# Optimization experiments

Measured on AMD Instinct MI355X. Metric: run time of the kernel, lower is better.

The kernel has to match this reference:

```python
import jax, jax.numpy as jnp
import numpy as np

N_EMBD = 1024
NUM_HEADS = 16
HEAD_SIZE = N_EMBD // NUM_HEADS
B, T = 2, 2048


def setup_inputs() -> dict:
    key = jax.random.key(0)
    k1, k2, k3, k4 = jax.random.split(key, 4)
    x = jax.random.normal(k1, (B, T, N_EMBD), dtype=jnp.float32)
    # torch nn.Linear weight is [out,in]; we store transposed [in,out] for x @ W
    w_qkv = jax.random.normal(k2, (N_EMBD, 3 * N_EMBD), dtype=jnp.float32) * (N_EMBD ** -0.5)
    w_proj = jax.random.normal(k3, (N_EMBD, N_EMBD), dtype=jnp.float32) * (N_EMBD ** -0.5)
    b_proj = jax.random.normal(k4, (N_EMBD,), dtype=jnp.float32) * 0.01
    return {"x": x, "w_qkv": w_qkv, "w_proj": w_proj, "b_proj": b_proj}


def reference(x, w_qkv, w_proj, b_proj):
    Bm, Tm, C = x.shape
    H, D = NUM_HEADS, HEAD_SIZE
    qkv = x @ w_qkv  # [B,T,3C]
    # einops 'b t (h d three) -> three b h t d': 'three' is the innermost factor
    qkv = qkv.reshape(Bm, Tm, H, D, 3)
    q = qkv[..., 0].transpose(0, 2, 1, 3)  # [B,H,T,D]
    k = qkv[..., 1].transpose(0, 2, 1, 3)
    v = qkv[..., 2].transpose(0, 2, 1, 3)
    scale = D ** -0.5
    attn = jnp.einsum('bhqd,bhkd->bhqk', q, k) * scale  # [B,H,T,T]
    causal_mask = jnp.triu(jnp.ones((Tm, Tm), dtype=bool), k=1)
    attn = jnp.where(causal_mask, -jnp.inf, attn)
    attn = jax.nn.softmax(attn, axis=-1)
    out = jnp.einsum('bhqk,bhkd->bhqd', attn, v)  # [B,H,T,D]
    out = out.transpose(0, 2, 1, 3).reshape(Bm, Tm, C)  # b h t d -> b t (h d)
    out = out @ w_proj + b_proj
    return out
```

## Files before the change

kernel.cpp:

```cpp
#include <hip/hip_runtime.h>
#include <hip/hip_bf16.h>
#include <math.h>

typedef __bf16 bf16x8 __attribute__((ext_vector_type(8)));
typedef __bf16 bf16x4 __attribute__((ext_vector_type(4)));
typedef float f32x4 __attribute__((ext_vector_type(4)));

#define MFMA16(A, B, C) __builtin_amdgcn_mfma_f32_16x16x32_bf16(A, B, C, 0, 0, 0)

__device__ __forceinline__ void cp16(void* lds_base, const void* g) {
  __builtin_amdgcn_global_load_lds(
      (const __attribute__((address_space(1))) void*)g,
      (__attribute__((address_space(3))) void*)lds_base, 16, 0, 0);
}

static constexpr int Bc   = 2;
static constexpr int Tc   = 2048;
static constexpr int Cc   = 1024;
static constexpr int Hc   = 16;
static constexpr int Dc   = 64;
static constexpr int Mrows = Bc * Tc;
static constexpr int N3    = 3 * Cc;

__global__ __launch_bounds__(256) void convert_x(
    const float* __restrict__ src, __bf16* __restrict__ dst, int n) {
  const int i0 = (blockIdx.x * 256 + threadIdx.x) * 8;
  if (i0 >= n) return;
  f32x4 a = *(const f32x4*)(src + i0);
  f32x4 b = *(const f32x4*)(src + i0 + 4);
  bf16x8 v;
#pragma unroll
  for (int j = 0; j < 4; ++j) { v[j] = (__bf16)a[j]; v[4 + j] = (__bf16)b[j]; }
  *(bf16x8*)(dst + i0) = v;
}

__global__ __launch_bounds__(256) void transpose_weights(
    const float* __restrict__ wqkv, const float* __restrict__ wproj,
    __bf16* __restrict__ dqkv, __bf16* __restrict__ dproj) {
  __shared__ __bf16 tile[32][33];
  const bool isproj = blockIdx.x >= 96;
  const float* src = isproj ? wproj : wqkv;
  __bf16* dst = isproj ? dproj : dqkv;
  const int N = isproj ? Cc : N3;
  const int K = Cc;
  const int n0 = (isproj ? (blockIdx.x - 96) : blockIdx.x) * 32;
  const int k0 = blockIdx.y * 32;
  const int x = threadIdx.x & 31;
  const int y = threadIdx.x >> 5;
  {
    int n = n0 + x;
    int col = n;
    if (!isproj) {
      int three = n >> 10, rem = n & 1023;
      int h = rem >> 6, d = rem & 63;
      col = h * 192 + d * 3 + three;
    }
#pragma unroll
    for (int r = 0; r < 4; ++r) {
      int k = k0 + y + r * 8;
      tile[y + r * 8][x] = (__bf16)src[(size_t)k * N + col];
    }
  }
  __syncthreads();
#pragma unroll
  for (int r = 0; r < 4; ++r) {
    int n = n0 + y + r * 8;
    dst[(size_t)n * K + k0 + x] = tile[x][y + r * 8];
  }
}

__global__ __launch_bounds__(256) void v_transpose(
    const __bf16* __restrict__ qkvp, __bf16* __restrict__ vt) {
  __shared__ __bf16 tile[32][33];
  const int t0 = blockIdx.x * 32;
  const int d0 = blockIdx.y * 32;
  const int bh = blockIdx.z;
  const int b = bh >> 4, h = bh & 15;
  const int x = threadIdx.x & 31;
  const int y = threadIdx.x >> 5;
#pragma unroll
  for (int r = 0; r < 4; ++r) {
    int t = t0 + y + r * 8;
    tile[y + r * 8][x] =
        qkvp[(size_t)(b * Tc + t) * N3 + 2 * Cc + h * 64 + d0 + x];
  }
  __syncthreads();
#pragma unroll
  for (int r = 0; r < 4; ++r) {
    int d = d0 + y + r * 8;
    vt[((size_t)bh * 64 + d) * Tc + t0 + x] = tile[x][y + r * 8];
  }
}

template <bool F32OUT>
__global__ __launch_bounds__(256) void gemm_nt(
    const __bf16* __restrict__ A, const __bf16* __restrict__ Bt,
    void* __restrict__ Cmat, const float* __restrict__ bias,
    int M, int N, int K, int ldc) {
  __shared__ __align__(16) __bf16 As[128 * 64];
  __shared__ __align__(16) __bf16 Bs[128 * 64];
  const int n0 = blockIdx.x * 128, m0 = blockIdx.y * 128;
  const int tid = threadIdx.x;
  const int wave = tid >> 6, lane = tid & 63;
  const int quad = lane >> 4, l16 = lane & 15;
  const int wm = (wave >> 1) * 64, wn = (wave & 1) * 64;
  const int srow = lane >> 3;
  const int scol = (((lane & 7) ^ (srow & 7))) * 8;

  f32x4 acc[4][4] = {};

  for (int k0 = 0; k0 < K; k0 += 64) {
    __syncthreads();
#pragma unroll
    for (int c = 0; c < 4; ++c) {
      int rowblk = c * 4 + wave;
      int row = rowblk * 8 + srow;
      cp16(&As[rowblk * 512], A + (size_t)(m0 + row) * K + k0 + scol);
      cp16(&Bs[rowblk * 512], Bt + (size_t)(n0 + row) * K + k0 + scol);
    }
    __syncthreads();
#pragma unroll
    for (int kk = 0; kk < 64; kk += 32) {
      bf16x8 af[4], bfr[4];
#pragma unroll
      for (int i = 0; i < 4; ++i) {
        int chunk = (((kk >> 3) + quad) ^ (l16 & 7)) * 8;
        af[i]  = *(const bf16x8*)(&As[(wm + i * 16 + l16) * 64 + chunk]);
        bfr[i] = *(const bf16x8*)(&Bs[(wn + i * 16 + l16) * 64 + chunk]);
      }
#pragma unroll
      for (int mi = 0; mi < 4; ++mi)
#pragma unroll
        for (int ni = 0; ni < 4; ++ni)
          acc[mi][ni] = MFMA16(af[mi], bfr[ni], acc[mi][ni]);
    }
  }

#pragma unroll
  for (int ni = 0; ni < 4; ++ni) {
    int col = n0 + wn + ni * 16 + l16;
    float bv = bias ? bias[col] : 0.0f;
#pragma unroll
    for (int mi = 0; mi < 4; ++mi)
#pragma unroll
      for (int r = 0; r < 4; ++r) {
        int row = m0 + wm + mi * 16 + quad * 4 + r;
        float v = acc[mi][ni][r] + bv;
        if (F32OUT)
          ((float*)Cmat)[(size_t)row * ldc + col] = v;
        else
          ((__bf16*)Cmat)[(size_t)row * ldc + col] = (__bf16)v;
      }
  }
}

#define LOG2E 1.44269504088896340736f
#define C2SC  (0.125f * LOG2E)
#define SH2   (16.0f * LOG2E)
static constexpr int LPK = 72;
static constexpr int LPV = 136;
static constexpr int TB  = 128;

__global__ __launch_bounds__(512, 4) void attn_kernel(
    const __bf16* __restrict__ qkv,
    const __bf16* __restrict__ vt,
    __bf16* __restrict__ obuf) {
  __shared__ __align__(16) __bf16 Ks[TB * LPK];
  __shared__ __align__(16) __bf16 Vs[64 * LPV];
  __shared__ __align__(16) __bf16 plds[8][16 * LPK];

  const int bh = blockIdx.x;
  const int pairidx = blockIdx.y;
  const int b = bh >> 4, hh = bh & 15;
  const int tid = threadIdx.x;
  const int wave = tid >> 6, lane = tid & 63;
  const int quad = lane >> 4, l16 = lane & 15;

  const __bf16* qbase = qkv + (size_t)(b * Tc) * N3 + hh * 64;
  const __bf16* kbase = qbase + Cc;
  const __bf16* vtb = vt + (size_t)bh * 64 * Tc;

  const int krow = tid >> 2;
  const int kcol = (tid & 3) * 16;
  const int vrow = tid >> 3;
  const int vcol = (tid & 7) * 16;

#pragma unroll
  for (int pi = 0; pi < 2; ++pi) {
    const int qt = pi ? (15 - pairidx) : pairidx;
    const int q0 = qt * 128;
    const int qb = q0 + wave * 16;
    const int kblocks = q0 + 128;

    bf16x8 bQ[2];
    {
      const __bf16* qr = qbase + (size_t)(qb + l16) * N3;
      bQ[0] = *(const bf16x8*)(qr + quad * 8);
      bQ[1] = *(const bf16x8*)(qr + 32 + quad * 8);
    }

    f32x4 accO[4] = {};
    float l_part = 0.0f;

    bf16x8 kp[2], vp[2];
    {
      const __bf16* kr = kbase + (size_t)krow * N3 + kcol;
      const __bf16* vr = vtb + (size_t)vrow * Tc + vcol;
#pragma unroll
      for (int j = 0; j < 2; ++j) {
        kp[j] = *(const bf16x8*)(kr + j * 8);
        vp[j] = *(const bf16x8*)(vr + j * 8);
      }
    }

    for (int kc = 0; kc < kblocks; kc += TB) {
      __syncthreads();
#pragma unroll
      for (int j = 0; j < 2; ++j) {
        *(bf16x8*)(&Ks[krow * LPK + kcol + j * 8]) = kp[j];
        *(bf16x8*)(&Vs[vrow * LPV + vcol + j * 8]) = vp[j];
      }
      if (kc + TB < kblocks) {
        const __bf16* kr = kbase + (size_t)(kc + TB + krow) * N3 + kcol;
        const __bf16* vr = vtb + (size_t)vrow * Tc + kc + TB + vcol;
#pragma unroll
        for (int j = 0; j < 2; ++j) {
          kp[j] = *(const bf16x8*)(kr + j * 8);
          vp[j] = *(const bf16x8*)(vr + j * 8);
        }
      }
      __syncthreads();

#pragma unroll
      for (int sub = 0; sub < 2; ++sub) {
        const int kc2 = kc + sub * 64;
        if (kc2 >= qb + 16) continue;

        f32x4 st[4];
        __builtin_amdgcn_s_setprio(1);
#pragma unroll
        for (int kt = 0; kt < 4; ++kt) {
          const int trow = sub * 64 + kt * 16 + l16;
          bf16x8 kf0 = *(const bf16x8*)(&Ks[trow * LPK + quad * 8]);
          bf16x8 kf1 = *(const bf16x8*)(&Ks[trow * LPK + 32 + quad * 8]);
          f32x4 a = {};
          a = MFMA16(kf0, bQ[0], a);
          a = MFMA16(kf1, bQ[1], a);
          st[kt] = a;
        }
        __builtin_amdgcn_s_setprio(0);
        if (kc2 + 64 > qb) {
          int qcol = qb + l16;
#pragma unroll
          for (int kt = 0; kt < 4; ++kt)
#pragma unroll
            for (int r = 0; r < 4; ++r) {
              int t = kc2 + kt * 16 + quad * 4 + r;
              if (t > qcol) st[kt][r] = -INFINITY;
            }
        }
#pragma unroll
        for (int kt = 0; kt < 4; ++kt)
#pragma unroll
          for (int r = 0; r < 4; ++r) {
            float p = __builtin_amdgcn_exp2f(fmaf(st[kt][r], C2SC, -SH2));
            st[kt][r] = p;
            l_part += p;
          }
#pragma unroll
        for (int kt = 0; kt < 4; ++kt) {
          bf16x4 pv;
#pragma unroll
          for (int r = 0; r < 4; ++r) pv[r] = (__bf16)st[kt][r];
          *(bf16x4*)(&plds[wave][l16 * LPK + kt * 16 + quad * 4]) = pv;
        }
        __threadfence_block();
        bf16x8 bP[2];
        bP[0] = *(const bf16x8*)(&plds[wave][l16 * LPK + quad * 8]);
        bP[1] = *(const bf16x8*)(&plds[wave][l16 * LPK + 32 + quad * 8]);
        __builtin_amdgcn_s_setprio(1);
#pragma unroll
        for (int dt = 0; dt < 4; ++dt) {
          const int drow = (dt * 16 + l16) * LPV + sub * 64;
          bf16x8 vf0 = *(const bf16x8*)(&Vs[drow + quad * 8]);
          bf16x8 vf1 = *(const bf16x8*)(&Vs[drow + 32 + quad * 8]);
          accO[dt] = MFMA16(vf0, bP[0], accO[dt]);
          accO[dt] = MFMA16(vf1, bP[1], accO[dt]);
        }
        __builtin_amdgcn_s_setprio(0);
      }
    }

    {
      float l_i = l_part;
      l_i += __shfl_xor(l_i, 16);
      l_i += __shfl_xor(l_i, 32);
      float inv = 1.0f / l_i;
      __bf16* orow = obuf + (size_t)(b * Tc + qb + l16) * Cc + hh * 64;
#pragma unroll
      for (int dt = 0; dt < 4; ++dt) {
        bf16x4 ov;
#pragma unroll
        for (int r = 0; r < 4; ++r) ov[r] = (__bf16)(accO[dt][r] * inv);
        *(bf16x4*)(orow + dt * 16 + quad * 4) = ov;
      }
    }
  }
}

extern "C" void kernel_launch(void* const* d_in, const int* in_sizes, int n_in,
                              void* d_out, int out_size, void* d_ws, size_t ws_size,
                              hipStream_t stream) {
  const float* x      = (const float*)d_in[0];
  const float* w_qkv  = (const float*)d_in[1];
  const float* w_proj = (const float*)d_in[2];
  const float* b_proj = (const float*)d_in[3];

  bool f32out = true;
  {
    size_t out_bytes = 0;
    if (hipMemPtrGetInfo(d_out, &out_bytes) == hipSuccess && out_bytes != 0)
      f32out = out_bytes >= (size_t)out_size * 4;
  }

  __bf16* xb     = (__bf16*)d_ws;
  __bf16* wqkvT  = xb + (size_t)Mrows * Cc;
  __bf16* wprojT = wqkvT + (size_t)N3 * Cc;
  __bf16* qkvp   = wprojT + (size_t)Cc * Cc;
  __bf16* vt     = qkvp + (size_t)Mrows * N3;
  __bf16* obuf   = vt + (size_t)Bc * Hc * Dc * Tc;

  convert_x<<<(Mrows * Cc) / (256 * 8), 256, 0, stream>>>(x, xb, Mrows * Cc);
  transpose_weights<<<dim3(128, 32), 256, 0, stream>>>(
      w_qkv, w_proj, wqkvT, wprojT);
  gemm_nt<false><<<dim3(N3 / 128, Mrows / 128), 256, 0, stream>>>(
      xb, wqkvT, qkvp, nullptr, Mrows, N3, Cc, N3);
  v_transpose<<<dim3(Tc / 32, 2, Bc * Hc), 256, 0, stream>>>(qkvp, vt);
  attn_kernel<<<dim3(Bc * Hc, 8), 512, 0, stream>>>(qkvp, vt, obuf);
  if (f32out) {
    gemm_nt<true><<<dim3(Cc / 128, Mrows / 128), 256, 0, stream>>>(
        obuf, wprojT, d_out, b_proj, Mrows, Cc, Cc, Cc);
  } else {
    gemm_nt<false><<<dim3(Cc / 128, Mrows / 128), 256, 0, stream>>>(
        obuf, wprojT, d_out, b_proj, Mrows, Cc, Cc, Cc);
  }
}
```

Before: 177.7 us.

## Merge input conversion and weight transpose into one prep kernel; move attention barrier

Fuses the x-to-bf16 conversion and the weight transpose/permute kernels into a single launch by splitting the 1D grid into two block ranges, removing one kernel launch and its gap. In the attention kernel, the second barrier now sits right after the LDS stores, before the global prefetch of the next K/V tile. This makes the prefetch loads issue after the barrier instead of before it. The barrier moves may change how global-load latency overlaps with compute.

After: 181.7 us. 2.2% more time.

```diff
diff --git a/kernel.cpp b/kernel.cpp
--- a/kernel.cpp
+++ b/kernel.cpp
@@ -22,33 +22,35 @@
 static constexpr int Mrows = Bc * Tc;
 static constexpr int N3    = 3 * Cc;
 
-__global__ __launch_bounds__(256) void convert_x(
-    const float* __restrict__ src, __bf16* __restrict__ dst, int n) {
-  const int i0 = (blockIdx.x * 256 + threadIdx.x) * 8;
-  if (i0 >= n) return;
-  f32x4 a = *(const f32x4*)(src + i0);
-  f32x4 b = *(const f32x4*)(src + i0 + 4);
-  bf16x8 v;
-#pragma unroll
-  for (int j = 0; j < 4; ++j) { v[j] = (__bf16)a[j]; v[4 + j] = (__bf16)b[j]; }
-  *(bf16x8*)(dst + i0) = v;
-}
-
-__global__ __launch_bounds__(256) void transpose_weights(
-    const float* __restrict__ wqkv, const float* __restrict__ wproj,
+__global__ __launch_bounds__(256) void prep_kernel(
+    const float* __restrict__ x, const float* __restrict__ wqkv,
+    const float* __restrict__ wproj, __bf16* __restrict__ xb,
     __bf16* __restrict__ dqkv, __bf16* __restrict__ dproj) {
+  if (blockIdx.x < 2048) {
+    const int i0 = (blockIdx.x * 256 + threadIdx.x) * 8;
+    f32x4 a = *(const f32x4*)(x + i0);
+    f32x4 b = *(const f32x4*)(x + i0 + 4);
+    bf16x8 v;
+#pragma unroll
+    for (int j = 0; j < 4; ++j) { v[j] = (__bf16)a[j]; v[4 + j] = (__bf16)b[j]; }
+    *(bf16x8*)(xb + i0) = v;
+    return;
+  }
   __shared__ __bf16 tile[32][33];
-  const bool isproj = blockIdx.x >= 96;
+  const int idx2 = blockIdx.x - 2048;
+  const int bx = idx2 & 127;
+  const int by = idx2 >> 7;
+  const bool isproj = bx >= 96;
   const float* src = isproj ? wproj : wqkv;
   __bf16* dst = isproj ? dproj : dqkv;
   const int N = isproj ? Cc : N3;
   const int K = Cc;
-  const int n0 = (isproj ? (blockIdx.x - 96) : blockIdx.x) * 32;
-  const int k0 = blockIdx.y * 32;
-  const int x = threadIdx.x & 31;
+  const int n0 = (isproj ? (bx - 96) : bx) * 32;
+  const int k0 = by * 32;
+  const int xx = threadIdx.x & 31;
   const int y = threadIdx.x >> 5;
   {
-    int n = n0 + x;
+    int n = n0 + xx;
     int col = n;
     if (!isproj) {
       int three = n >> 10, rem = n & 1023;
@@ -58,14 +60,14 @@
 #pragma unroll
     for (int r = 0; r < 4; ++r) {
       int k = k0 + y + r * 8;
-      tile[y + r * 8][x] = (__bf16)src[(size_t)k * N + col];
+      tile[y + r * 8][xx] = (__bf16)src[(size_t)k * N + col];
     }
   }
   __syncthreads();
 #pragma unroll
   for (int r = 0; r < 4; ++r) {
     int n = n0 + y + r * 8;
-    dst[(size_t)n * K + k0 + x] = tile[x][y + r * 8];
+    dst[(size_t)n * K + k0 + xx] = tile[xx][y + r * 8];
   }
 }
 
@@ -220,6 +222,8 @@
         *(bf16x8*)(&Ks[krow * LPK + kcol + j * 8]) = kp[j];
         *(bf16x8*)(&Vs[vrow * LPV + vcol + j * 8]) = vp[j];
       }
+      __syncthreads();
+
       if (kc + TB < kblocks) {
         const __bf16* kr = kbase + (size_t)(kc + TB + krow) * N3 + kcol;
         const __bf16* vr = vtb + (size_t)vrow * Tc + kc + TB + vcol;
@@ -229,7 +233,6 @@
           vp[j] = *(const bf16x8*)(vr + j * 8);
         }
       }
-      __syncthreads();
 
 #pragma unroll
       for (int sub = 0; sub < 2; ++sub) {
@@ -330,9 +333,8 @@
   __bf16* vt     = qkvp + (size_t)Mrows * N3;
   __bf16* obuf   = vt + (size_t)Bc * Hc * Dc * Tc;
 
-  convert_x<<<(Mrows * Cc) / (256 * 8), 256, 0, stream>>>(x, xb, Mrows * Cc);
-  transpose_weights<<<dim3(128, 32), 256, 0, stream>>>(
-      w_qkv, w_proj, wqkvT, wprojT);
+  prep_kernel<<<2048 + 4096, 256, 0, stream>>>(
+      x, w_qkv, w_proj, xb, wqkvT, wprojT);
   gemm_nt<false><<<dim3(N3 / 128, Mrows / 128), 256, 0, stream>>>(
       xb, wqkvT, qkvp, nullptr, Mrows, N3, Cc, N3);
   v_transpose<<<dim3(Tc / 32, 2, Bc * Hc), 256, 0, stream>>>(qkvp, vt);
```
